# Optimization experiments

Hardware: AMD Instinct MI355X
Metric: run time of the kernel (lower is better)

The kernel has to match this reference:

```python
import jax, jax.numpy as jnp
import numpy as np

E, R, B, S, D = 8, 64, 4, 4096, 2048
SCALE = 1.0  # alpha / rank = 64/64


def setup_inputs() -> dict:
    key = jax.random.key(0)
    k1, k2, k3, k4 = jax.random.split(key, 4)
    x = jax.random.normal(k1, (B, S, D), dtype=jnp.float32)
    lora_A = jax.random.normal(k2, (E, R, D), dtype=jnp.float32) * 0.02  # [E, rank, in]
    lora_B = jax.random.normal(k3, (E, D, R), dtype=jnp.float32) * 0.02  # [E, out, rank]
    task_indices = jax.random.randint(k4, (B, S), 0, E)
    return {"x": x, "lora_A": lora_A, "lora_B": lora_B, "task_indices": task_indices}


def reference(x, lora_A, lora_B, task_indices):
    # Faithful to torch forward with task_indices: compute EVERY adapter's
    # low-rank output for all tokens, then mask by (task_indices == i) and sum.
    # adapter_i(x) = (x @ A_i^T) @ B_i^T * (alpha/rank)
    h = jnp.einsum('bsd,erd->bser', x, lora_A)            # [B,S,E,R] per-expert low-rank acts
    mask = jax.nn.one_hot(task_indices, lora_A.shape[0], dtype=x.dtype)  # [B,S,E]
    # Contract rank and expert dims with the mask; equivalent to sum_i mask_i * adapter_i(x)
    out = jnp.einsum('bser,edr,bse->bsd', h, lora_B, mask) * SCALE
    return out
```

## Files before the change

kernel.cpp:

```cpp
#include <hip/hip_runtime.h>

#define E_ 8
#define R_ 64
#define D_ 2048
#define BS_ 16384
#define SEG 64
#define WS_ABF_OFF (1ull<<20)
#define WS_NEED_FULL (WS_ABF_OFF + 4ull*1024*1024)

typedef __attribute__((ext_vector_type(8))) short short8;
typedef __attribute__((ext_vector_type(4))) short short4v;
typedef __attribute__((ext_vector_type(4))) float f32x4;
typedef __attribute__((ext_vector_type(2))) unsigned int u32x2;

__device__ __forceinline__ unsigned short f2bf(float f){
  unsigned u = __float_as_uint(f);
  u += 0x7fffu + ((u >> 16) & 1u);
  return (unsigned short)(u >> 16);
}
__device__ __forceinline__ short8 pack8(f32x4 a, f32x4 b){
  short8 r;
  r[0]=(short)f2bf(a[0]); r[1]=(short)f2bf(a[1]); r[2]=(short)f2bf(a[2]); r[3]=(short)f2bf(a[3]);
  r[4]=(short)f2bf(b[0]); r[5]=(short)f2bf(b[1]); r[6]=(short)f2bf(b[2]); r[7]=(short)f2bf(b[3]);
  return r;
}
__device__ __forceinline__ void gload16(const void* g, void* l){
  __builtin_amdgcn_global_load_lds(
      (const __attribute__((address_space(1))) void*)g,
      (__attribute__((address_space(3))) void*)l, 16, 0, 0);
}

__global__ void scatter_conv(const int* __restrict__ tidx, int* __restrict__ ws,
                             const float* __restrict__ Am, const float* __restrict__ Bm,
                             unsigned short* __restrict__ Abf){
  if (blockIdx.x >= 64){
    const int i = (blockIdx.x - 64)*256 + threadIdx.x;
    const f32x4 v = (i < 262144) ? *(const f32x4*)(Am + (size_t)i*4)
                                 : *(const f32x4*)(Bm + (size_t)(i - 262144)*4);
    short4v a;
    a[0]=(short)f2bf(v[0]); a[1]=(short)f2bf(v[1]); a[2]=(short)f2bf(v[2]); a[3]=(short)f2bf(v[3]);
    *(short4v*)(Abf + (size_t)i*4) = a;
    return;
  }
  __shared__ int lh[E_], lbase[E_], lrank[E_];
  const int t = threadIdx.x;
  if (t < E_){ lh[t] = 0; lrank[t] = 0; }
  __syncthreads();
  const int tok = blockIdx.x*256 + t;
  const int e = tidx[tok];
  atomicAdd(&lh[e], 1);
  __syncthreads();
  if (t < E_) lbase[t] = atomicAdd(&ws[t], lh[t]);
  __syncthreads();
  const int r = atomicAdd(&lrank[e], 1);
  ws[SEG + e*BS_ + lbase[e] + r] = tok;
}

__global__ __launch_bounds__(256) void fused(
    const float* __restrict__ x, const unsigned short* __restrict__ Abf,
    const int* __restrict__ ws, float* __restrict__ out)
{
  const int e    = blockIdx.x & 7;
  const int tile = blockIdx.x >> 3;
  const int cnt  = ws[e];
  const int start = tile * 32;
  if (start >= cnt) return;
  const int valid = (cnt - start < 32) ? (cnt - start) : 32;
  const int* seg = ws + SEG + e*BS_;

  __shared__ int tokIds[32];
  __shared__ __align__(16) char smem[36864];

  const int tid = threadIdx.x;
  if (tid < 32) tokIds[tid] = seg[start + (tid < valid ? tid : valid-1)];
  __syncthreads();

  const int lane = tid & 63, w = tid >> 6;
  const char* xsrc[4]; const char* asrc[4];
  #pragma unroll
  for (int i = 0; i < 4; ++i){
    const int gi = w*4 + i;
    const int xrow = gi*2 + (lane >> 5);
    xsrc[i] = (const char*)(x + (size_t)tokIds[xrow]*D_)
              + (((lane & 31)*16) ^ ((xrow & 7) << 4));
    const int arow = gi*4 + (lane >> 4);
    asrc[i] = (const char*)(Abf + ((size_t)e*R_ + arow)*D_)
              + (((lane & 15)*16) ^ ((arow & 7) << 4));
  }
  char* xdst = smem;
  char* adst = smem + 16384;
  char* pH   = smem + 32768;

  const int llo = lane & 15, lhi = lane >> 4;
  const int tw = w & 1, rw = w >> 1;
  const int xrow_c = tw*16 + llo;
  const int arow0  = rw*32 + llo;
  const int sw     = (llo & 7) << 4;
  f32x4 acc0={0.f,0.f,0.f,0.f}, acc1={0.f,0.f,0.f,0.f};

  for (int c = 0; c < 16; ++c){
    #pragma unroll
    for (int i = 0; i < 4; ++i){
      gload16(xsrc[i] + c*512, xdst + (w*4+i)*1024);
      gload16(asrc[i] + c*256, adst + (w*4+i)*1024);
    }
    __syncthreads();
    #pragma unroll
    for (int kk = 0; kk < 4; ++kk){
      const f32x4 v0 = *(const f32x4*)(xdst + xrow_c*512 + ((kk*128 + lhi*32) ^ sw));
      const f32x4 v1 = *(const f32x4*)(xdst + xrow_c*512 + ((kk*128 + lhi*32 + 16) ^ sw));
      const short8 af = pack8(v0, v1);
      const short8 b0 = *(const short8*)(adst + arow0*256 + ((kk*64 + lhi*16) ^ sw));
      const short8 b1 = *(const short8*)(adst + (arow0+16)*256 + ((kk*64 + lhi*16) ^ sw));
      acc0 = __builtin_amdgcn_mfma_f32_16x16x32_bf16(af, b0, acc0, 0,0,0);
      acc1 = __builtin_amdgcn_mfma_f32_16x16x32_bf16(af, b1, acc1, 0,0,0);
    }
    __syncthreads();
  }

  #pragma unroll
  for (int i = 0; i < 4; ++i){
    const int hr = tw*16 + lhi*4 + i;
    const int hsw = (hr & 7) << 4;
    *(unsigned short*)(pH + ((hr*128 + (rw*32+llo)*2)    ^ hsw)) = f2bf(acc0[i]);
    *(unsigned short*)(pH + ((hr*128 + (rw*32+16+llo)*2) ^ hsw)) = f2bf(acc1[i]);
  }
  __syncthreads();

  short8 aH[2][2];
  #pragma unroll
  for (int g = 0; g < 2; ++g){
    const int r_ = g*16 + llo;
    aH[g][0] = *(const short8*)(pH + ((r_*128 + lhi*16) ^ sw));
    aH[g][1] = *(const short8*)(pH + ((r_*128 + 64 + lhi*16) ^ sw));
  }

  unsigned vmask = 0;
  int rowOff[2][4];
  #pragma unroll
  for (int g = 0; g < 2; ++g){
    #pragma unroll
    for (int i = 0; i < 4; ++i){
      const int r_ = g*16 + lhi*4 + i;
      if (r_ < valid) vmask |= 1u << (g*4 + i);
      rowOff[g][i] = tokIds[r_ < valid ? r_ : 0]*D_ + llo;
    }
  }

  const unsigned short* Bbf = Abf + E_*R_*D_;
  const char* bsrc = (const char*)Bbf + (size_t)e*D_*R_*2
                     + (size_t)(w*64 + (lane >> 3))*128
                     + (((lane & 7)*16) ^ (((lane >> 3) & 7) << 4));
  char* pB = smem;

  for (int cg = 0; cg < 8; ++cg){
    #pragma unroll
    for (int i2 = 0; i2 < 8; ++i2)
      gload16(bsrc + cg*32768 + i2*1024, pB + (w*8+i2)*1024);
    __syncthreads();
    #pragma unroll
    for (int nt = 0; nt < 4; ++nt){
      const int rowL = w*64 + nt*16 + llo;
      const short8 b0 = *(const short8*)(pB + ((rowL*128 + lhi*16) ^ sw));
      const short8 b1 = *(const short8*)(pB + ((rowL*128 + 64 + lhi*16) ^ sw));
      f32x4 o0 = {0.f,0.f,0.f,0.f}, o1 = {0.f,0.f,0.f,0.f};
      o0 = __builtin_amdgcn_mfma_f32_16x16x32_bf16(aH[0][0], b0, o0, 0,0,0);
      o0 = __builtin_amdgcn_mfma_f32_16x16x32_bf16(aH[0][1], b1, o0, 0,0,0);
      o1 = __builtin_amdgcn_mfma_f32_16x16x32_bf16(aH[1][0], b0, o1, 0,0,0);
      o1 = __builtin_amdgcn_mfma_f32_16x16x32_bf16(aH[1][1], b1, o1, 0,0,0);
      const int col = cg*256 + w*64 + nt*16;
      #pragma unroll
      for (int i = 0; i < 4; ++i){
        if (vmask & (1u <<  i))    __builtin_nontemporal_store(o0[i], &out[rowOff[0][i] + col]);
        if (vmask & (1u << (4+i))) __builtin_nontemporal_store(o1[i], &out[rowOff[1][i] + col]);
      }
    }
    __syncthreads();
  }
}

__global__ __launch_bounds__(256) void naive_kernel(
    const float* __restrict__ x, const float* __restrict__ Am,
    const float* __restrict__ Bm, const int* __restrict__ tidx,
    float* __restrict__ out)
{
  const int tok = blockIdx.x;
  const int e = tidx[tok];
  __shared__ float xs[D_];
  __shared__ float h[R_];
  const int tid = threadIdx.x;
  for (int i = tid; i < D_; i += 256) xs[i] = x[(size_t)tok*D_ + i];
  __syncthreads();
  if (tid < R_){
    float s = 0.f;
    const float* ar = Am + ((size_t)e*R_ + tid)*D_;
    for (int d = 0; d < D_; ++d) s += xs[d]*ar[d];
    h[tid] = s;
  }
  __syncthreads();
  for (int c = tid; c < D_; c += 256){
    float s = 0.f;
    const float* br = Bm + ((size_t)e*D_ + c)*R_;
    #pragma unroll
    for (int r = 0; r < R_; ++r) s += h[r]*br[r];
    out[(size_t)tok*D_ + c] = s;
  }
}

extern "C" void kernel_launch(void* const* d_in, const int* in_sizes, int n_in,
                              void* d_out, int out_size, void* d_ws, size_t ws_size,
                              hipStream_t stream){
  const float* x    = (const float*)d_in[0];
  const float* Am   = (const float*)d_in[1];
  const float* Bm   = (const float*)d_in[2];
  const int*   tidx = (const int*)d_in[3];
  float* out = (float*)d_out;
  int*   ws  = (int*)d_ws;
  unsigned short* Abf = (unsigned short*)((char*)d_ws + WS_ABF_OFF);

  if (ws_size >= WS_NEED_FULL){
    hipMemsetAsync(d_ws, 0, 32, stream);
    scatter_conv<<<64 + 2048, 256, 0, stream>>>(tidx, ws, Am, Bm, Abf);
    fused<<<8*(BS_/32), 256, 0, stream>>>(x, Abf, ws, out);
  } else {
    naive_kernel<<<BS_, 256, 0, stream>>>(x, Am, Bm, tidx, out);
  }
}
```

Before: 80.66 us.

## Double-buffer LDS staging in both GEMM phases with manual waitcnt barriers

```diff
diff --git a/kernel.cpp b/kernel.cpp
--- a/kernel.cpp
+++ b/kernel.cpp
@@ -11,7 +11,6 @@
 typedef __attribute__((ext_vector_type(8))) short short8;
 typedef __attribute__((ext_vector_type(4))) short short4v;
 typedef __attribute__((ext_vector_type(4))) float f32x4;
-typedef __attribute__((ext_vector_type(2))) unsigned int u32x2;
 
 __device__ __forceinline__ unsigned short f2bf(float f){
   unsigned u = __float_as_uint(f);
@@ -69,7 +68,7 @@
   const int* seg = ws + SEG + e*BS_;
 
   __shared__ int tokIds[32];
-  __shared__ __align__(16) char smem[36864];
+  __shared__ __align__(16) char smem[69632];
 
   const int tid = threadIdx.x;
   if (tid < 32) tokIds[tid] = seg[start + (tid < valid ? tid : valid-1)];
@@ -87,9 +86,7 @@
     asrc[i] = (const char*)(Abf + ((size_t)e*R_ + arow)*D_)
               + (((lane & 15)*16) ^ ((arow & 7) << 4));
   }
-  char* xdst = smem;
-  char* adst = smem + 16384;
-  char* pH   = smem + 32768;
+  char* const pH = smem + 65536;
 
   const int llo = lane & 15, lhi = lane >> 4;
   const int tw = w & 1, rw = w >> 1;
@@ -98,25 +95,66 @@
   const int sw     = (llo & 7) << 4;
   f32x4 acc0={0.f,0.f,0.f,0.f}, acc1={0.f,0.f,0.f,0.f};
 
-  for (int c = 0; c < 16; ++c){
+  auto STAGE = [&](int c, int buf){
+    char* xd = smem + buf*16384;
+    char* ad = smem + 32768 + buf*16384;
     #pragma unroll
     for (int i = 0; i < 4; ++i){
-      gload16(xsrc[i] + c*512, xdst + (w*4+i)*1024);
-      gload16(asrc[i] + c*256, adst + (w*4+i)*1024);
-    }
-    __syncthreads();
+      gload16(xsrc[i] + c*512, xd + (w*4+i)*1024);
+      gload16(asrc[i] + c*256, ad + (w*4+i)*1024);
+    }
+  };
+  auto COMPUTE = [&](int buf){
+    const char* xd = smem + buf*16384;
+    const char* ad = smem + 32768 + buf*16384;
     #pragma unroll
     for (int kk = 0; kk < 4; ++kk){
-      const f32x4 v0 = *(const f32x4*)(xdst + xrow_c*512 + ((kk*128 + lhi*32) ^ sw));
-      const f32x4 v1 = *(const f32x4*)(xdst + xrow_c*512 + ((kk*128 + lhi*32 + 16) ^ sw));
+      const f32x4 v0 = *(const f32x4*)(xd + xrow_c*512 + ((kk*128 + lhi*32) ^ sw));
+      const f32x4 v1 = *(const f32x4*)(xd + xrow_c*512 + ((kk*128 + lhi*32 + 16) ^ sw));
       const short8 af = pack8(v0, v1);
-      const short8 b0 = *(const short8*)(adst + arow0*256 + ((kk*64 + lhi*16) ^ sw));
-      const short8 b1 = *(const short8*)(adst + (arow0+16)*256 + ((kk*64 + lhi*16) ^ sw));
+      const short8 b0 = *(const short8*)(ad + arow0*256 + ((kk*64 + lhi*16) ^ sw));
+      const short8 b1 = *(const short8*)(ad + (arow0+16)*256 + ((kk*64 + lhi*16) ^ sw));
       acc0 = __builtin_amdgcn_mfma_f32_16x16x32_bf16(af, b0, acc0, 0,0,0);
       acc1 = __builtin_amdgcn_mfma_f32_16x16x32_bf16(af, b1, acc1, 0,0,0);
     }
-    __syncthreads();
-  }
+  };
+  auto PSTEP = [&](int c, int buf){
+    STAGE(c+1, buf^1);
+    asm volatile("s_waitcnt vmcnt(8)" ::: "memory");
+    __builtin_amdgcn_s_barrier();
+    asm volatile("" ::: "memory");
+    COMPUTE(buf);
+    __builtin_amdgcn_sched_barrier(0);
+    __builtin_amdgcn_s_barrier();
+    asm volatile("" ::: "memory");
+  };
+
+  STAGE(0, 0);
+  #pragma unroll 1
+  for (int c2 = 0; c2 < 7; ++c2){
+    PSTEP(c2*2,     0);
+    PSTEP(c2*2 + 1, 1);
+  }
+  PSTEP(14, 0);
+  asm volatile("s_waitcnt vmcnt(0)" ::: "memory");
+  __builtin_amdgcn_s_barrier();
+  asm volatile("" ::: "memory");
+  COMPUTE(1);
+  __builtin_amdgcn_sched_barrier(0);
+  __builtin_amdgcn_s_barrier();
+  asm volatile("" ::: "memory");
+
+  const unsigned short* Bbf = Abf + E_*R_*D_;
+  const char* bsrc = (const char*)Bbf + (size_t)e*D_*R_*2
+                     + (size_t)(w*64 + (lane >> 3))*128
+                     + (((lane & 7)*16) ^ (((lane >> 3) & 7) << 4));
+  auto STAGE_B = [&](int cg, int buf){
+    char* pb = smem + buf*32768;
+    #pragma unroll
+    for (int i2 = 0; i2 < 8; ++i2)
+      gload16(bsrc + cg*32768 + i2*1024, pb + (w*8+i2)*1024);
+  };
+  STAGE_B(0, 0);
 
   #pragma unroll
   for (int i = 0; i < 4; ++i){
@@ -125,7 +163,9 @@
     *(unsigned short*)(pH + ((hr*128 + (rw*32+llo)*2)    ^ hsw)) = f2bf(acc0[i]);
     *(unsigned short*)(pH + ((hr*128 + (rw*32+16+llo)*2) ^ hsw)) = f2bf(acc1[i]);
   }
-  __syncthreads();
+  asm volatile("s_waitcnt lgkmcnt(0)" ::: "memory");
+  __builtin_amdgcn_s_barrier();
+  asm volatile("" ::: "memory");
 
   short8 aH[2][2];
   #pragma unroll
@@ -147,22 +187,21 @@
     }
   }
 
-  const unsigned short* Bbf = Abf + E_*R_*D_;
-  const char* bsrc = (const char*)Bbf + (size_t)e*D_*R_*2
-                     + (size_t)(w*64 + (lane >> 3))*128
-                     + (((lane & 7)*16) ^ (((lane >> 3) & 7) << 4));
-  char* pB = smem;
-
-  for (int cg = 0; cg < 8; ++cg){
-    #pragma unroll
-    for (int i2 = 0; i2 < 8; ++i2)
-      gload16(bsrc + cg*32768 + i2*1024, pB + (w*8+i2)*1024);
-    __syncthreads();
+  auto BSTEP = [&](int cg, int buf, bool last){
+    if (!last){
+      STAGE_B(cg+1, buf^1);
+      asm volatile("s_waitcnt vmcnt(8)" ::: "memory");
+    } else {
+      asm volatile("s_waitcnt vmcnt(0)" ::: "memory");
+    }
+    __builtin_amdgcn_s_barrier();
+    asm volatile("" ::: "memory");
+    const char* pb = smem + buf*32768;
     #pragma unroll
     for (int nt = 0; nt < 4; ++nt){
       const int rowL = w*64 + nt*16 + llo;
-      const short8 b0 = *(const short8*)(pB + ((rowL*128 + lhi*16) ^ sw));
-      const short8 b1 = *(const short8*)(pB + ((rowL*128 + 64 + lhi*16) ^ sw));
+      const short8 b0 = *(const short8*)(pb + ((rowL*128 + lhi*16) ^ sw));
+      const short8 b1 = *(const short8*)(pb + ((rowL*128 + 64 + lhi*16) ^ sw));
       f32x4 o0 = {0.f,0.f,0.f,0.f}, o1 = {0.f,0.f,0.f,0.f};
       o0 = __builtin_amdgcn_mfma_f32_16x16x32_bf16(aH[0][0], b0, o0, 0,0,0);
       o0 = __builtin_amdgcn_mfma_f32_16x16x32_bf16(aH[0][1], b1, o0, 0,0,0);
@@ -175,8 +214,14 @@
         if (vmask & (1u << (4+i))) __builtin_nontemporal_store(o1[i], &out[rowOff[1][i] + col]);
       }
     }
-    __syncthreads();
-  }
+    if (!last){
+      __builtin_amdgcn_sched_barrier(0);
+      __builtin_amdgcn_s_barrier();
+      asm volatile("" ::: "memory");
+    }
+  };
+  BSTEP(0,0,false); BSTEP(1,1,false); BSTEP(2,0,false); BSTEP(3,1,false);
+  BSTEP(4,0,false); BSTEP(5,1,false); BSTEP(6,0,false); BSTEP(7,1,true);
 }
 
 __global__ __launch_bounds__(256) void naive_kernel(
```

After: 101.5 us. 1.26x slower.

## Split fused LoRA kernel into split-K down-projection and column-split up-projection stages

Applied to the files above, without the earlier changes.

```diff
diff --git a/kernel.cpp b/kernel.cpp
--- a/kernel.cpp
+++ b/kernel.cpp
@@ -6,12 +6,14 @@
 #define BS_ 16384
 #define SEG 64
 #define WS_ABF_OFF (1ull<<20)
-#define WS_NEED_FULL (WS_ABF_OFF + 4ull*1024*1024)
+#define WS_HP_OFF  (WS_ABF_OFF + 4ull*1024*1024)
+#define WS_NEED_FULL (WS_HP_OFF + 16ull*1024*1024)
+#define NTILE 128
+#define KSLICE_F (BS_*R_)
 
 typedef __attribute__((ext_vector_type(8))) short short8;
 typedef __attribute__((ext_vector_type(4))) short short4v;
 typedef __attribute__((ext_vector_type(4))) float f32x4;
-typedef __attribute__((ext_vector_type(2))) unsigned int u32x2;
 
 __device__ __forceinline__ unsigned short f2bf(float f){
   unsigned u = __float_as_uint(f);
@@ -56,12 +58,13 @@
   ws[SEG + e*BS_ + lbase[e] + r] = tok;
 }
 
-__global__ __launch_bounds__(256) void fused(
+__global__ __launch_bounds__(256) void stage1(
     const float* __restrict__ x, const unsigned short* __restrict__ Abf,
-    const int* __restrict__ ws, float* __restrict__ out)
+    const int* __restrict__ ws, float* __restrict__ Hp)
 {
   const int e    = blockIdx.x & 7;
-  const int tile = blockIdx.x >> 3;
+  const int tile = (blockIdx.x >> 3) & (NTILE-1);
+  const int ks   = blockIdx.x >> 10;
   const int cnt  = ws[e];
   const int start = tile * 32;
   if (start >= cnt) return;
@@ -69,7 +72,7 @@
   const int* seg = ws + SEG + e*BS_;
 
   __shared__ int tokIds[32];
-  __shared__ __align__(16) char smem[36864];
+  __shared__ __align__(16) char smem[32768];
 
   const int tid = threadIdx.x;
   if (tid < 32) tokIds[tid] = seg[start + (tid < valid ? tid : valid-1)];
@@ -87,9 +90,8 @@
     asrc[i] = (const char*)(Abf + ((size_t)e*R_ + arow)*D_)
               + (((lane & 15)*16) ^ ((arow & 7) << 4));
   }
-  char* xdst = smem;
-  char* adst = smem + 16384;
-  char* pH   = smem + 32768;
+  char* const xdst = smem;
+  char* const adst = smem + 16384;
 
   const int llo = lane & 15, lhi = lane >> 4;
   const int tw = w & 1, rw = w >> 1;
@@ -98,7 +100,10 @@
   const int sw     = (llo & 7) << 4;
   f32x4 acc0={0.f,0.f,0.f,0.f}, acc1={0.f,0.f,0.f,0.f};
 
-  for (int c = 0; c < 16; ++c){
+  const int cbase = ks*4;
+  #pragma unroll
+  for (int cc = 0; cc < 4; ++cc){
+    const int c = cbase + cc;
     #pragma unroll
     for (int i = 0; i < 4; ++i){
       gload16(xsrc[i] + c*512, xdst + (w*4+i)*1024);
@@ -118,13 +123,60 @@
     __syncthreads();
   }
 
+  float* const hks = Hp + (size_t)ks*KSLICE_F;
   #pragma unroll
   for (int i = 0; i < 4; ++i){
     const int hr = tw*16 + lhi*4 + i;
-    const int hsw = (hr & 7) << 4;
-    *(unsigned short*)(pH + ((hr*128 + (rw*32+llo)*2)    ^ hsw)) = f2bf(acc0[i]);
-    *(unsigned short*)(pH + ((hr*128 + (rw*32+16+llo)*2) ^ hsw)) = f2bf(acc1[i]);
-  }
+    float* hrow = hks + (size_t)tokIds[hr]*R_;
+    hrow[rw*32 + llo]      = acc0[i];
+    hrow[rw*32 + 16 + llo] = acc1[i];
+  }
+}
+
+__global__ __launch_bounds__(256) void stage2(
+    const unsigned short* __restrict__ Abf, const float* __restrict__ Hp,
+    const int* __restrict__ ws, float* __restrict__ out)
+{
+  const int e    = blockIdx.x & 7;
+  const int tile = (blockIdx.x >> 3) & (NTILE-1);
+  const int cg   = blockIdx.x >> 10;
+  const int cnt  = ws[e];
+  const int start = tile * 32;
+  if (start >= cnt) return;
+  const int valid = (cnt - start < 32) ? (cnt - start) : 32;
+  const int* seg = ws + SEG + e*BS_;
+
+  __shared__ int tokIds[32];
+  __shared__ __align__(16) char smem[36864];
+
+  const int tid = threadIdx.x;
+  if (tid < 32) tokIds[tid] = seg[start + (tid < valid ? tid : valid-1)];
+
+  const int lane = tid & 63, w = tid >> 6;
+  const int llo = lane & 15, lhi = lane >> 4;
+  const int sw  = (llo & 7) << 4;
+  char* const pB = smem;
+  char* const pH = smem + 32768;
+
+  const unsigned short* Bbf = Abf + E_*R_*D_;
+  const char* bsrc = (const char*)Bbf + (size_t)e*D_*R_*2 + (size_t)cg*32768
+                     + (size_t)(w*64 + (lane >> 3))*128
+                     + (((lane & 7)*16) ^ (((lane >> 3) & 7) << 4));
+  #pragma unroll
+  for (int i2 = 0; i2 < 8; ++i2)
+    gload16(bsrc + i2*1024, pB + (w*8+i2)*1024);
+
+  const int hrow = tid >> 3;
+  const int tokH = seg[start + (hrow < valid ? hrow : valid-1)];
+  const float* hp = Hp + (size_t)tokH*R_ + (tid & 7)*8;
+  f32x4 s0 = {0.f,0.f,0.f,0.f}, s1 = {0.f,0.f,0.f,0.f};
+  #pragma unroll
+  for (int k2 = 0; k2 < 4; ++k2){
+    s0 += *(const f32x4*)(hp + (size_t)k2*KSLICE_F);
+    s1 += *(const f32x4*)(hp + (size_t)k2*KSLICE_F + 4);
+  }
+  const int hc = (tid & 7)*8;
+  *(short8*)(pH + ((hrow*128 + hc*2) ^ ((hrow & 7) << 4))) = pack8(s0, s1);
   __syncthreads();
 
   short8 aH[2][2];
@@ -147,35 +199,22 @@
     }
   }
 
-  const unsigned short* Bbf = Abf + E_*R_*D_;
-  const char* bsrc = (const char*)Bbf + (size_t)e*D_*R_*2
-                     + (size_t)(w*64 + (lane >> 3))*128
-                     + (((lane & 7)*16) ^ (((lane >> 3) & 7) << 4));
-  char* pB = smem;
-
-  for (int cg = 0; cg < 8; ++cg){
-    #pragma unroll
-    for (int i2 = 0; i2 < 8; ++i2)
-      gload16(bsrc + cg*32768 + i2*1024, pB + (w*8+i2)*1024);
-    __syncthreads();
-    #pragma unroll
-    for (int nt = 0; nt < 4; ++nt){
-      const int rowL = w*64 + nt*16 + llo;
-      const short8 b0 = *(const short8*)(pB + ((rowL*128 + lhi*16) ^ sw));
-      const short8 b1 = *(const short8*)(pB + ((rowL*128 + 64 + lhi*16) ^ sw));
-      f32x4 o0 = {0.f,0.f,0.f,0.f}, o1 = {0.f,0.f,0.f,0.f};
-      o0 = __builtin_amdgcn_mfma_f32_16x16x32_bf16(aH[0][0], b0, o0, 0,0,0);
-      o0 = __builtin_amdgcn_mfma_f32_16x16x32_bf16(aH[0][1], b1, o0, 0,0,0);
-      o1 = __builtin_amdgcn_mfma_f32_16x16x32_bf16(aH[1][0], b0, o1, 0,0,0);
-      o1 = __builtin_amdgcn_mfma_f32_16x16x32_bf16(aH[1][1], b1, o1, 0,0,0);
-      const int col = cg*256 + w*64 + nt*16;
-      #pragma unroll
-      for (int i = 0; i < 4; ++i){
-        if (vmask & (1u <<  i))    __builtin_nontemporal_store(o0[i], &out[rowOff[0][i] + col]);
-        if (vmask & (1u << (4+i))) __builtin_nontemporal_store(o1[i], &out[rowOff[1][i] + col]);
-      }
-    }
-    __syncthreads();
+  #pragma unroll
+  for (int nt = 0; nt < 4; ++nt){
+    const int rowL = w*64 + nt*16 + llo;
+    const short8 b0 = *(const short8*)(pB + ((rowL*128 + lhi*16) ^ sw));
+    const short8 b1 = *(const short8*)(pB + ((rowL*128 + 64 + lhi*16) ^ sw));
+    f32x4 o0 = {0.f,0.f,0.f,0.f}, o1 = {0.f,0.f,0.f,0.f};
+    o0 = __builtin_amdgcn_mfma_f32_16x16x32_bf16(aH[0][0], b0, o0, 0,0,0);
+    o0 = __builtin_amdgcn_mfma_f32_16x16x32_bf16(aH[0][1], b1, o0, 0,0,0);
+    o1 = __builtin_amdgcn_mfma_f32_16x16x32_bf16(aH[1][0], b0, o1, 0,0,0);
+    o1 = __builtin_amdgcn_mfma_f32_16x16x32_bf16(aH[1][1], b1, o1, 0,0,0);
+    const int col = cg*256 + w*64 + nt*16;
+    #pragma unroll
+    for (int i = 0; i < 4; ++i){
+      if (vmask & (1u <<  i))    __builtin_nontemporal_store(o0[i], &out[rowOff[0][i] + col]);
+      if (vmask & (1u << (4+i))) __builtin_nontemporal_store(o1[i], &out[rowOff[1][i] + col]);
+    }
   }
 }
 
@@ -217,11 +256,13 @@
   float* out = (float*)d_out;
   int*   ws  = (int*)d_ws;
   unsigned short* Abf = (unsigned short*)((char*)d_ws + WS_ABF_OFF);
+  float* Hp = (float*)((char*)d_ws + WS_HP_OFF);
 
   if (ws_size >= WS_NEED_FULL){
     hipMemsetAsync(d_ws, 0, 32, stream);
     scatter_conv<<<64 + 2048, 256, 0, stream>>>(tidx, ws, Am, Bm, Abf);
-    fused<<<8*(BS_/32), 256, 0, stream>>>(x, Abf, ws, out);
+    stage1<<<4*8*NTILE, 256, 0, stream>>>(x, Abf, ws, Hp);
+    stage2<<<8*8*NTILE, 256, 0, stream>>>(Abf, Hp, ws, out);
   } else {
     naive_kernel<<<BS_, 256, 0, stream>>>(x, Am, Bm, tidx, out);
   }
```

After: 87.45 us. +8.4%, slower.

## Shrink token tiles to 16 and load operands directly from global memory

Applied to the files above, without the earlier changes.

```diff
diff --git a/kernel.cpp b/kernel.cpp
--- a/kernel.cpp
+++ b/kernel.cpp
@@ -7,11 +7,11 @@
 #define SEG 64
 #define WS_ABF_OFF (1ull<<20)
 #define WS_NEED_FULL (WS_ABF_OFF + 4ull*1024*1024)
+#define NTILE 512
 
 typedef __attribute__((ext_vector_type(8))) short short8;
 typedef __attribute__((ext_vector_type(4))) short short4v;
 typedef __attribute__((ext_vector_type(4))) float f32x4;
-typedef __attribute__((ext_vector_type(2))) unsigned int u32x2;
 
 __device__ __forceinline__ unsigned short f2bf(float f){
   unsigned u = __float_as_uint(f);
@@ -23,11 +23,6 @@
   r[0]=(short)f2bf(a[0]); r[1]=(short)f2bf(a[1]); r[2]=(short)f2bf(a[2]); r[3]=(short)f2bf(a[3]);
   r[4]=(short)f2bf(b[0]); r[5]=(short)f2bf(b[1]); r[6]=(short)f2bf(b[2]); r[7]=(short)f2bf(b[3]);
   return r;
-}
-__device__ __forceinline__ void gload16(const void* g, void* l){
-  __builtin_amdgcn_global_load_lds(
-      (const __attribute__((address_space(1))) void*)g,
-      (__attribute__((address_space(3))) void*)l, 16, 0, 0);
 }
 
 __global__ void scatter_conv(const int* __restrict__ tidx, int* __restrict__ ws,
@@ -56,126 +51,79 @@
   ws[SEG + e*BS_ + lbase[e] + r] = tok;
 }
 
-__global__ __launch_bounds__(256) void fused(
+__global__ __launch_bounds__(256, 4) void fused16(
     const float* __restrict__ x, const unsigned short* __restrict__ Abf,
     const int* __restrict__ ws, float* __restrict__ out)
 {
   const int e    = blockIdx.x & 7;
   const int tile = blockIdx.x >> 3;
   const int cnt  = ws[e];
-  const int start = tile * 32;
+  const int start = tile * 16;
   if (start >= cnt) return;
-  const int valid = (cnt - start < 32) ? (cnt - start) : 32;
+  const int valid = (cnt - start < 16) ? (cnt - start) : 16;
   const int* seg = ws + SEG + e*BS_;
 
-  __shared__ int tokIds[32];
-  __shared__ __align__(16) char smem[36864];
+  __shared__ int tokIds[16];
+  __shared__ __align__(16) char pH[2048];
 
   const int tid = threadIdx.x;
-  if (tid < 32) tokIds[tid] = seg[start + (tid < valid ? tid : valid-1)];
+  if (tid < 16) tokIds[tid] = seg[start + (tid < valid ? tid : valid-1)];
   __syncthreads();
 
   const int lane = tid & 63, w = tid >> 6;
-  const char* xsrc[4]; const char* asrc[4];
-  #pragma unroll
-  for (int i = 0; i < 4; ++i){
-    const int gi = w*4 + i;
-    const int xrow = gi*2 + (lane >> 5);
-    xsrc[i] = (const char*)(x + (size_t)tokIds[xrow]*D_)
-              + (((lane & 31)*16) ^ ((xrow & 7) << 4));
-    const int arow = gi*4 + (lane >> 4);
-    asrc[i] = (const char*)(Abf + ((size_t)e*R_ + arow)*D_)
-              + (((lane & 15)*16) ^ ((arow & 7) << 4));
-  }
-  char* xdst = smem;
-  char* adst = smem + 16384;
-  char* pH   = smem + 32768;
+  const int llo = lane & 15, lhi = lane >> 4;
+  const int sw  = (llo & 7) << 4;
 
-  const int llo = lane & 15, lhi = lane >> 4;
-  const int tw = w & 1, rw = w >> 1;
-  const int xrow_c = tw*16 + llo;
-  const int arow0  = rw*32 + llo;
-  const int sw     = (llo & 7) << 4;
-  f32x4 acc0={0.f,0.f,0.f,0.f}, acc1={0.f,0.f,0.f,0.f};
-
+  const float* px = x + (size_t)tokIds[llo]*D_ + lhi*8;
+  const unsigned short* pa = Abf + (size_t)(e*R_ + w*16 + llo)*D_ + lhi*8;
+  f32x4 acc = {0.f,0.f,0.f,0.f};
+  #pragma unroll 2
   for (int c = 0; c < 16; ++c){
     #pragma unroll
-    for (int i = 0; i < 4; ++i){
-      gload16(xsrc[i] + c*512, xdst + (w*4+i)*1024);
-      gload16(asrc[i] + c*256, adst + (w*4+i)*1024);
+    for (int kk = 0; kk < 4; ++kk){
+      const f32x4 v0 = *(const f32x4*)(px + c*128 + kk*32);
+      const f32x4 v1 = *(const f32x4*)(px + c*128 + kk*32 + 4);
+      const short8 b0 = *(const short8*)(pa + c*128 + kk*32);
+      acc = __builtin_amdgcn_mfma_f32_16x16x32_bf16(pack8(v0, v1), b0, acc, 0,0,0);
     }
-    __syncthreads();
-    #pragma unroll
-    for (int kk = 0; kk < 4; ++kk){
-      const f32x4 v0 = *(const f32x4*)(xdst + xrow_c*512 + ((kk*128 + lhi*32) ^ sw));
-      const f32x4 v1 = *(const f32x4*)(xdst + xrow_c*512 + ((kk*128 + lhi*32 + 16) ^ sw));
-      const short8 af = pack8(v0, v1);
-      const short8 b0 = *(const short8*)(adst + arow0*256 + ((kk*64 + lhi*16) ^ sw));
-      const short8 b1 = *(const short8*)(adst + (arow0+16)*256 + ((kk*64 + lhi*16) ^ sw));
-      acc0 = __builtin_amdgcn_mfma_f32_16x16x32_bf16(af, b0, acc0, 0,0,0);
-      acc1 = __builtin_amdgcn_mfma_f32_16x16x32_bf16(af, b1, acc1, 0,0,0);
-    }
-    __syncthreads();
   }
 
   #pragma unroll
   for (int i = 0; i < 4; ++i){
-    const int hr = tw*16 + lhi*4 + i;
-    const int hsw = (hr & 7) << 4;
-    *(unsigned short*)(pH + ((hr*128 + (rw*32+llo)*2)    ^ hsw)) = f2bf(acc0[i]);
-    *(unsigned short*)(pH + ((hr*128 + (rw*32+16+llo)*2) ^ hsw)) = f2bf(acc1[i]);
+    const int hr = lhi*4 + i;
+    *(unsigned short*)(pH + ((hr*128 + (w*16 + llo)*2) ^ ((hr & 7) << 4))) = f2bf(acc[i]);
   }
   __syncthreads();
 
-  short8 aH[2][2];
-  #pragma unroll
-  for (int g = 0; g < 2; ++g){
-    const int r_ = g*16 + llo;
-    aH[g][0] = *(const short8*)(pH + ((r_*128 + lhi*16) ^ sw));
-    aH[g][1] = *(const short8*)(pH + ((r_*128 + 64 + lhi*16) ^ sw));
-  }
+  const short8 aH0 = *(const short8*)(pH + ((llo*128 + lhi*16) ^ sw));
+  const short8 aH1 = *(const short8*)(pH + ((llo*128 + 64 + lhi*16) ^ sw));
 
   unsigned vmask = 0;
-  int rowOff[2][4];
+  int rowOff[4];
   #pragma unroll
-  for (int g = 0; g < 2; ++g){
-    #pragma unroll
-    for (int i = 0; i < 4; ++i){
-      const int r_ = g*16 + lhi*4 + i;
-      if (r_ < valid) vmask |= 1u << (g*4 + i);
-      rowOff[g][i] = tokIds[r_ < valid ? r_ : 0]*D_ + llo;
-    }
+  for (int i = 0; i < 4; ++i){
+    const int r_ = lhi*4 + i;
+    if (r_ < valid) vmask |= 1u << i;
+    rowOff[i] = tokIds[r_ < valid ? r_ : 0]*D_ + llo;
   }
 
   const unsigned short* Bbf = Abf + E_*R_*D_;
-  const char* bsrc = (const char*)Bbf + (size_t)e*D_*R_*2
-                     + (size_t)(w*64 + (lane >> 3))*128
-                     + (((lane & 7)*16) ^ (((lane >> 3) & 7) << 4));
-  char* pB = smem;
-
+  const unsigned short* pb = Bbf + (size_t)e*D_*R_ + (size_t)(w*64 + llo)*R_ + lhi*8;
+  #pragma unroll 2
   for (int cg = 0; cg < 8; ++cg){
     #pragma unroll
-    for (int i2 = 0; i2 < 8; ++i2)
-      gload16(bsrc + cg*32768 + i2*1024, pB + (w*8+i2)*1024);
-    __syncthreads();
-    #pragma unroll
     for (int nt = 0; nt < 4; ++nt){
-      const int rowL = w*64 + nt*16 + llo;
-      const short8 b0 = *(const short8*)(pB + ((rowL*128 + lhi*16) ^ sw));
-      const short8 b1 = *(const short8*)(pB + ((rowL*128 + 64 + lhi*16) ^ sw));
-      f32x4 o0 = {0.f,0.f,0.f,0.f}, o1 = {0.f,0.f,0.f,0.f};
-      o0 = __builtin_amdgcn_mfma_f32_16x16x32_bf16(aH[0][0], b0, o0, 0,0,0);
-      o0 = __builtin_amdgcn_mfma_f32_16x16x32_bf16(aH[0][1], b1, o0, 0,0,0);
-      o1 = __builtin_amdgcn_mfma_f32_16x16x32_bf16(aH[1][0], b0, o1, 0,0,0);
-      o1 = __builtin_amdgcn_mfma_f32_16x16x32_bf16(aH[1][1], b1, o1, 0,0,0);
+      const short8 b0 = *(const short8*)(pb + cg*16384 + nt*1024);
+      const short8 b1 = *(const short8*)(pb + cg*16384 + nt*1024 + 32);
+      f32x4 o = {0.f,0.f,0.f,0.f};
+      o = __builtin_amdgcn_mfma_f32_16x16x32_bf16(aH0, b0, o, 0,0,0);
+      o = __builtin_amdgcn_mfma_f32_16x16x32_bf16(aH1, b1, o, 0,0,0);
       const int col = cg*256 + w*64 + nt*16;
       #pragma unroll
-      for (int i = 0; i < 4; ++i){
-        if (vmask & (1u <<  i))    __builtin_nontemporal_store(o0[i], &out[rowOff[0][i] + col]);
-        if (vmask & (1u << (4+i))) __builtin_nontemporal_store(o1[i], &out[rowOff[1][i] + col]);
-      }
+      for (int i = 0; i < 4; ++i)
+        if (vmask & (1u << i))
+          __builtin_nontemporal_store(o[i], &out[rowOff[i] + col]);
     }
-    __syncthreads();
   }
 }
 
@@ -221,7 +169,7 @@
   if (ws_size >= WS_NEED_FULL){
     hipMemsetAsync(d_ws, 0, 32, stream);
     scatter_conv<<<64 + 2048, 256, 0, stream>>>(tidx, ws, Am, Bm, Abf);
-    fused<<<8*(BS_/32), 256, 0, stream>>>(x, Abf, ws, out);
+    fused16<<<8*NTILE, 256, 0, stream>>>(x, Abf, ws, out);
   } else {
     naive_kernel<<<BS_, 256, 0, stream>>>(x, Am, Bm, tidx, out);
   }
```

Result: slower. 164.2 us (+103.6%).
